# Optimization experiments

Hardware: AMD Instinct MI355X
Metric: run time of the kernel (lower is better)

The kernel has to match this reference:

```python
import jax, jax.numpy as jnp
import numpy as np

N = 2048          # num_nodes
A = 100           # anchor count (hard-coded in _select_anchor_points)


def setup_inputs() -> dict:
    key = jax.random.key(0)
    k1, k2, k3 = jax.random.split(key, 3)
    motifGraph = jax.random.uniform(k1, (N, N), dtype=jnp.float32)
    node_weights = jax.random.uniform(k2, (N,), dtype=jnp.float32)
    weight_matrix = jax.random.uniform(k3, (N, A), dtype=jnp.float32)
    sigma = jnp.array(1.0, dtype=jnp.float32)
    return {"motifGraph": motifGraph, "node_weights": node_weights,
            "weight_matrix": weight_matrix, "sigma": sigma}


def _floyd_warshall(w):
    # w: [n,n] edge-weight matrix (inf = no edge, 0 on diagonal)
    n = w.shape[0]
    def step(d, k):
        # d_ij = min(d_ij, d_ik + d_kj)
        d = jnp.minimum(d, d[:, k][:, None] + d[k, :][None, :])
        return d, None
    d, _ = jax.lax.scan(step, w, jnp.arange(n))
    return d


def reference(motifGraph, node_weights, weight_matrix, sigma):
    n = motifGraph.shape[0]
    # _adjust_motif_graph: row-scale by node weights. The original detaches
    # before the scipy floyd_warshall call, so no grad flows through it.
    adj = jax.lax.stop_gradient(motifGraph * node_weights[:n, None])
    # csr_matrix semantics: zero entries are "no edge"; directed=False takes
    # the min of w_ij and w_ji; diagonal distance is 0.
    w = jnp.where(adj > 0, adj, jnp.inf)
    w = jnp.minimum(w, w.T)
    idx = jnp.arange(n)
    w = w.at[idx, idx].set(0.0)
    dist = _floyd_warshall(w)
    dist = jnp.where(jnp.isinf(dist), 100.0, dist)
    # _select_anchor_points: top-100 node weights (all indices < n here)
    anchors = jnp.argsort(-jax.lax.stop_gradient(node_weights))[:A]
    consensus_vectors = dist[:, anchors]                      # [n, A]
    distance_sums = (consensus_vectors.sum(axis=1) - 100.0).sum() / (n * A)
    weighted = weight_matrix[:n, :] * consensus_vectors       # [n, A]
    # build_consensus_graph: cdist(...)**4 == (squared euclidean dist)**2
    xx = jnp.sum(weighted * weighted, axis=1)                 # [n]
    sq = jnp.maximum(xx[:, None] + xx[None, :] - 2.0 * weighted @ weighted.T, 0.0)
    consensus_graph = jnp.exp(-(sq * sq) / (2.0 * sigma ** 2))
    return consensus_vectors, distance_sums, consensus_graph
```

## Files before the change

### kernel.cpp

```cpp
#include <hip/hip_runtime.h>
#include <stdint.h>

#define NN 2048
#define AA 100
#define NT 32

#define F_DIAG 256
#define F_ROW  512
#define F_COL  1536

typedef float floatx4 __attribute__((ext_vector_type(4)));

template<bool AL> __device__ __forceinline__ float4 ld4(const float* __restrict__ p) {
  if (AL) return *(const float4*)p;
  return make_float4(p[0], p[1], p[2], p[3]);
}
template<bool AL> __device__ __forceinline__ void st4(float* __restrict__ p, float4 v) {
  if (AL) { *(float4*)p = v; }
  else { p[0] = v.x; p[1] = v.y; p[2] = v.z; p[3] = v.w; }
}

__device__ __forceinline__ void minplus16(const float (*A)[68], const float (*B)[68],
                                          float c[4][4], int i0, int j0) {
#pragma unroll 4
  for (int k4 = 0; k4 < 16; ++k4) {
    const int k = k4 * 4;
    float4 a0 = *(const float4*)&A[i0 + 0][k];
    float4 a1 = *(const float4*)&A[i0 + 1][k];
    float4 a2 = *(const float4*)&A[i0 + 2][k];
    float4 a3 = *(const float4*)&A[i0 + 3][k];
    float4 b0 = *(const float4*)&B[k + 0][j0];
    float4 b1 = *(const float4*)&B[k + 1][j0];
    float4 b2 = *(const float4*)&B[k + 2][j0];
    float4 b3 = *(const float4*)&B[k + 3][j0];
#define MP1(ii, jj, f)                                                           \
    c[ii][jj] = fminf(fminf(fminf(fminf(c[ii][jj], a##ii.x + b0.f),              \
                                  a##ii.y + b1.f),                               \
                            a##ii.z + b2.f),                                     \
                      a##ii.w + b3.f)
#define MP_ROW(ii) MP1(ii, 0, x); MP1(ii, 1, y); MP1(ii, 2, z); MP1(ii, 3, w)
    MP_ROW(0); MP_ROW(1); MP_ROW(2); MP_ROW(3);
#undef MP_ROW
#undef MP1
  }
}

__device__ __forceinline__ void close_seq(float (*S)[68], float c[4][4],
                                          int i0, int j0, int ty, int tx) {
  for (int kb = 0; kb < 16; ++kb) {
#pragma unroll
    for (int h = 0; h < 2; ++h) {
      const int k = kb * 4 + h * 2;
      float4 br  = *(const float4*)&S[k][j0];
      float4 br2 = *(const float4*)&S[k + 1][j0];
      float dkk1 = S[k][k + 1];
      float dk1k = S[k + 1][k];
      float a0 = S[i0 + 0][k],     a1 = S[i0 + 1][k],
            a2 = S[i0 + 2][k],     a3 = S[i0 + 3][k];
      float e0 = S[i0 + 0][k + 1], e1 = S[i0 + 1][k + 1],
            e2 = S[i0 + 2][k + 1], e3 = S[i0 + 3][k + 1];
      float4 brp;
      brp.x = fminf(br2.x, dk1k + br.x);
      brp.y = fminf(br2.y, dk1k + br.y);
      brp.z = fminf(br2.z, dk1k + br.z);
      brp.w = fminf(br2.w, dk1k + br.w);
      e0 = fminf(e0, a0 + dkk1);
      e1 = fminf(e1, a1 + dkk1);
      e2 = fminf(e2, a2 + dkk1);
      e3 = fminf(e3, a3 + dkk1);
#define CS2(ii, aa, ee)                                                     \
      c[ii][0] = fminf(fminf(c[ii][0], aa + br.x), ee + brp.x);             \
      c[ii][1] = fminf(fminf(c[ii][1], aa + br.y), ee + brp.y);             \
      c[ii][2] = fminf(fminf(c[ii][2], aa + br.z), ee + brp.z);             \
      c[ii][3] = fminf(fminf(c[ii][3], aa + br.w), ee + brp.w)
      CS2(0, a0, e0); CS2(1, a1, e1); CS2(2, a2, e2); CS2(3, a3, e3);
#undef CS2
      const int kn = k + 2;
      if (kn < 64) {
        const int ow = kn >> 2;
        const int ri = (h == 0) ? 2 : 0;
        if (ow == ty) {
          *(float4*)&S[kn][j0] =
              make_float4(c[ri][0], c[ri][1], c[ri][2], c[ri][3]);
          *(float4*)&S[kn + 1][j0] =
              make_float4(c[ri + 1][0], c[ri + 1][1], c[ri + 1][2], c[ri + 1][3]);
        }
        if (ow == tx) {
          S[i0 + 0][kn] = c[0][ri]; S[i0 + 0][kn + 1] = c[0][ri + 1];
          S[i0 + 1][kn] = c[1][ri]; S[i0 + 1][kn + 1] = c[1][ri + 1];
          S[i0 + 2][kn] = c[2][ri]; S[i0 + 2][kn + 1] = c[2][ri + 1];
          S[i0 + 3][kn] = c[3][ri]; S[i0 + 3][kn + 1] = c[3][ri + 1];
        }
      }
      __syncthreads();
    }
  }
}

template<int LAZY>
__device__ __forceinline__ void waitflag(int* f) {
  int it = 0;
  while (__hip_atomic_load(f, __ATOMIC_RELAXED, __HIP_MEMORY_SCOPE_AGENT) == 0) {
    if (++it > 24) __builtin_amdgcn_s_sleep(LAZY);
  }
}
__device__ __forceinline__ void setflag(int* f) {
  __hip_atomic_store(f, 1, __ATOMIC_RELAXED, __HIP_MEMORY_SCOPE_AGENT);
}

__device__ __forceinline__ void stage64(const float* __restrict__ g,
                                        float (*S)[68], int t) {
#pragma unroll
  for (int l = 0; l < 4; ++l) {
    int idx = l * 256 + t;
    int row = idx >> 4, c4 = (idx & 15) * 4;
    *(float4*)&S[row][c4] = *(const float4*)&g[row * 64 + c4];
  }
}
__device__ __forceinline__ void pub64_wt(float* __restrict__ g,
                                         const float c[4][4], int i0, int j0) {
#pragma unroll
  for (int ii = 0; ii < 4; ++ii) {
    floatx4 v = {c[ii][0], c[ii][1], c[ii][2], c[ii][3]};
    float* p = &g[(i0 + ii) * 64 + j0];
    asm volatile("global_store_dwordx4 %0, %1, off sc0 sc1"
                 :: "v"(p), "v"(v) : "memory");
  }
  asm volatile("s_waitcnt vmcnt(0)" ::: "memory");
}

__global__ __launch_bounds__(256, 4) void fw_persist(
    const float* __restrict__ mg, const float* __restrict__ nw,
    float* __restrict__ dist, int* __restrict__ Wi,
    float* __restrict__ diagb, float* __restrict__ rowb,
    float* __restrict__ colb) {
  __shared__ __align__(16) float As[64][68];
  __shared__ __align__(16) float Bs[64][68];
  const int bx = blockIdx.x, by = blockIdx.y;
  const int t = threadIdx.x;
  const int tx = t & 15, ty = t >> 4;
  const int i0 = ty * 4, j0 = tx * 4;
  int* DIAGF = Wi + F_DIAG;
  int* ROWF  = Wi + F_ROW;
  int* COLF  = Wi + F_COL;

#pragma unroll
  for (int l = 0; l < 4; ++l) {
    int idx = l * 256 + t;
    int r = idx >> 4, c4 = (idx & 15) * 4;
    float4 g = *(const float4*)&mg[(bx * 64 + r) * NN + by * 64 + c4];
    Bs[c4 + 0][r] = g.x; Bs[c4 + 1][r] = g.y;
    Bs[c4 + 2][r] = g.z; Bs[c4 + 3][r] = g.w;
  }
  __syncthreads();
  float c[4][4];
  {
    float4 nwj = *(const float4*)&nw[bx * 64 + j0];
#pragma unroll
    for (int ii = 0; ii < 4; ++ii) {
      int rl = i0 + ii;
      int i = by * 64 + rl;
      float nwi = nw[i];
      float4 m = *(const float4*)&mg[i * NN + bx * 64 + j0];
      float4 bt = *(const float4*)&Bs[rl][j0];
      float av[4] = {m.x * nwi, m.y * nwi, m.z * nwi, m.w * nwi};
      float bv[4] = {bt.x * nwj.x, bt.y * nwj.y, bt.z * nwj.z, bt.w * nwj.w};
#pragma unroll
      for (int q = 0; q < 4; ++q) {
        float wa = av[q] > 0.0f ? av[q] : __builtin_huge_valf();
        float wb = bv[q] > 0.0f ? bv[q] : __builtin_huge_valf();
        float v = fminf(wa, wb);
        if (i == bx * 64 + j0 + q) v = 0.0f;
        c[ii][q] = v;
      }
    }
  }
  if (bx == 0 && by == 0) {
    __syncthreads();
#pragma unroll
    for (int ii = 0; ii < 4; ++ii)
      *(float4*)&As[i0 + ii][j0] = make_float4(c[ii][0], c[ii][1], c[ii][2], c[ii][3]);
    __syncthreads();
    close_seq(As, c, i0, j0, ty, tx);
    pub64_wt(diagb, c, i0, j0);
    __syncthreads();
    if (t == 0) setflag(DIAGF + 0);
  }

  for (int r = 0; r < NT; ++r) {
    const bool crit = (by == r) || (bx == r) || (by == r + 1) || (bx == r + 1);
    if (crit) __builtin_amdgcn_s_setprio(1);
    else      __builtin_amdgcn_s_setprio(0);
    if (by == r && bx == r) continue;
    if (by == r || bx == r) {
      const bool isRow = (by == r);
      __syncthreads();
      float (*Ow)[68] = isRow ? Bs : As;
#pragma unroll
      for (int ii = 0; ii < 4; ++ii)
        *(float4*)&Ow[i0 + ii][j0] =
            make_float4(c[ii][0], c[ii][1], c[ii][2], c[ii][3]);
      if (t == 0) waitflag<1>(DIAGF + r);
      __syncthreads();
      stage64(diagb + r * 4096, isRow ? As : Bs, t);
      __syncthreads();
      minplus16(As, Bs, c, i0, j0);
      float* ob = isRow ? rowb + (r * NT + bx) * 4096
                        : colb + (by * NT + r) * 4096;
      pub64_wt(ob, c, i0, j0);
      __syncthreads();
      if (t == 0) setflag(isRow ? ROWF + r * NT + bx : COLF + by * NT + r);
    } else {
      const bool closer = (bx == r + 1) && (by == r + 1) && (r + 1 < NT);
      if (t == 0) {
        if (crit) {
          waitflag<1>(ROWF + r * NT + bx);
          waitflag<1>(COLF + by * NT + r);
        } else {
          waitflag<8>(ROWF + r * NT + bx);
          waitflag<8>(COLF + by * NT + r);
        }
      }
      __syncthreads();
      stage64(colb + (by * NT + r) * 4096, As, t);
      stage64(rowb + (r * NT + bx) * 4096, Bs, t);
      __syncthreads();
      minplus16(As, Bs, c, i0, j0);
      if (closer) {
        __syncthreads();
#pragma unroll
        for (int ii = 0; ii < 4; ++ii)
          *(float4*)&As[i0 + ii][j0] =
              make_float4(c[ii][0], c[ii][1], c[ii][2], c[ii][3]);
        __syncthreads();
        close_seq(As, c, i0, j0, ty, tx);
        pub64_wt(diagb + (r + 1) * 4096, c, i0, j0);
        __syncthreads();
        if (t == 0) setflag(DIAGF + r + 1);
      }
    }
  }
  __builtin_amdgcn_s_setprio(0);

  float* ob = &dist[(by * 64) * NN + bx * 64];
#pragma unroll
  for (int ii = 0; ii < 4; ++ii)
    *(float4*)&ob[(i0 + ii) * NN + j0] =
        make_float4(c[ii][0], c[ii][1], c[ii][2], c[ii][3]);
}

template<bool AL>
__global__ __launch_bounds__(256) void build_w_kernel(
    const float* __restrict__ mg, const float* __restrict__ nw,
    float* __restrict__ w) {
  __shared__ float Tt[64][65];
  __shared__ __align__(16) float As[64][68];
  int bi = blockIdx.y, bj = blockIdx.x;
  int t = threadIdx.x;
  const bool diag0 = (bi == 0) && (bj == 0);
#pragma unroll
  for (int l = 0; l < 4; ++l) {
    int idx = l * 256 + t;
    int r = idx >> 4, c4 = (idx & 15) * 4;
    float4 g = *(const float4*)&mg[(bj * 64 + r) * NN + bi * 64 + c4];
    Tt[c4 + 0][r] = g.x; Tt[c4 + 1][r] = g.y;
    Tt[c4 + 2][r] = g.z; Tt[c4 + 3][r] = g.w;
  }
  __syncthreads();
#pragma unroll
  for (int l = 0; l < 4; ++l) {
    int idx = l * 256 + t;
    int r = idx >> 4, c4 = (idx & 15) * 4;
    int i = bi * 64 + r, j = bj * 64 + c4;
    float4 m = *(const float4*)&mg[i * NN + j];
    float4 nwj = *(const float4*)&nw[j];
    float nwi = nw[i];
    float av[4] = {m.x * nwi, m.y * nwi, m.z * nwi, m.w * nwi};
    float bv[4] = {Tt[r][c4 + 0] * nwj.x, Tt[r][c4 + 1] * nwj.y,
                   Tt[r][c4 + 2] * nwj.z, Tt[r][c4 + 3] * nwj.w};
    float vv[4];
#pragma unroll
    for (int q = 0; q < 4; ++q) {
      float wa = av[q] > 0.0f ? av[q] : __builtin_huge_valf();
      float wb = bv[q] > 0.0f ? bv[q] : __builtin_huge_valf();
      float v = fminf(wa, wb);
      if (i == j + q) v = 0.0f;
      vv[q] = v;
    }
    float4 v4 = make_float4(vv[0], vv[1], vv[2], vv[3]);
    if (diag0) {
      *(float4*)&As[r][c4] = v4;
    } else {
      st4<AL>(&w[i * NN + j], v4);
    }
  }
  if (diag0) {
    __syncthreads();
    int tx = t & 15, ty = t >> 4;
    int i0 = ty * 4, j0 = tx * 4;
    float c[4][4];
#pragma unroll
    for (int ii = 0; ii < 4; ++ii) {
      float4 q = *(const float4*)&As[i0 + ii][j0];
      c[ii][0] = q.x; c[ii][1] = q.y; c[ii][2] = q.z; c[ii][3] = q.w;
    }
    close_seq(As, c, i0, j0, ty, tx);
#pragma unroll
    for (int ii = 0; ii < 4; ++ii)
      st4<AL>(&w[(i0 + ii) * NN + j0],
              make_float4(c[ii][0], c[ii][1], c[ii][2], c[ii][3]));
  }
}

template<bool AL>
__global__ __launch_bounds__(256) void fw_p2(float* __restrict__ d, int r) {
  __shared__ __align__(16) float As[64][68];
  __shared__ __align__(16) float Bs[64][68];
  int tile = blockIdx.x, side = blockIdx.y;
  if (tile == r) return;
  int t = threadIdx.x;
  int dbase = (r * 64) * NN + r * 64;
  int obase = (side == 0) ? (r * 64) * NN + tile * 64
                          : (tile * 64) * NN + r * 64;
  float (*Da)[68] = (side == 0) ? As : Bs;
  float (*Ow)[68] = (side == 0) ? Bs : As;
#pragma unroll
  for (int l = 0; l < 4; ++l) {
    int idx = l * 256 + t;
    int row = idx >> 4, c4 = (idx & 15) * 4;
    *(float4*)&Da[row][c4] = ld4<AL>(&d[dbase + row * NN + c4]);
    *(float4*)&Ow[row][c4] = ld4<AL>(&d[obase + row * NN + c4]);
  }
  int tx = t & 15, ty = t >> 4;
  int i0 = ty * 4, j0 = tx * 4;
  __syncthreads();
  float c[4][4];
#pragma unroll
  for (int ii = 0; ii < 4; ++ii) {
    float4 q = *(const float4*)&Ow[i0 + ii][j0];
    c[ii][0] = q.x; c[ii][1] = q.y; c[ii][2] = q.z; c[ii][3] = q.w;
  }
  minplus16(As, Bs, c, i0, j0);
#pragma unroll
  for (int ii = 0; ii < 4; ++ii)
    st4<AL>(&d[obase + (i0 + ii) * NN + j0],
            make_float4(c[ii][0], c[ii][1], c[ii][2], c[ii][3]));
}

template<bool AL>
__global__ __launch_bounds__(256) void fw_p3(float* __restrict__ d, int r) {
  __shared__ __align__(16) float As[64][68];
  __shared__ __align__(16) float Bs[64][68];
  int bx = blockIdx.x, by = blockIdx.y;
  if (bx == r || by == r) return;
  int t = threadIdx.x;
#pragma unroll
  for (int l = 0; l < 4; ++l) {
    int idx = l * 256 + t;
    int row = idx >> 4, c4 = (idx & 15) * 4;
    *(float4*)&As[row][c4] = ld4<AL>(&d[(by * 64 + row) * NN + r * 64 + c4]);
    *(float4*)&Bs[row][c4] = ld4<AL>(&d[(r * 64 + row) * NN + bx * 64 + c4]);
  }
  int tx = t & 15, ty = t >> 4;
  int i0 = ty * 4, j0 = tx * 4;
  int obase = (by * 64) * NN + bx * 64;
  float c[4][4];
#pragma unroll
  for (int ii = 0; ii < 4; ++ii) {
    float4 q = ld4<AL>(&d[obase + (i0 + ii) * NN + j0]);
    c[ii][0] = q.x; c[ii][1] = q.y; c[ii][2] = q.z; c[ii][3] = q.w;
  }
  __syncthreads();
  minplus16(As, Bs, c, i0, j0);

  bool closer = (bx == r + 1) && (by == r + 1) && (r + 1 < NT);
  if (closer) {
    __syncthreads();
#pragma unroll
    for (int ii = 0; ii < 4; ++ii)
      *(float4*)&As[i0 + ii][j0] = make_float4(c[ii][0], c[ii][1], c[ii][2], c[ii][3]);
    __syncthreads();
    close_seq(As, c, i0, j0, ty, tx);
  }
#pragma unroll
  for (int ii = 0; ii < 4; ++ii)
    st4<AL>(&d[obase + (i0 + ii) * NN + j0],
            make_float4(c[ii][0], c[ii][1], c[ii][2], c[ii][3]));
}

__global__ __launch_bounds__(256) void anchors_kernel(
    const float* __restrict__ nw, int* __restrict__ anchors) {
  __shared__ __align__(16) float s[NN];
  int t = threadIdx.x;
#pragma unroll
  for (int l = 0; l < NN / 256; ++l) s[l * 256 + t] = nw[l * 256 + t];
  __syncthreads();
  int i = blockIdx.x * 64 + (t >> 2);
  int q = t & 3;
  float wi = s[i];
  int rank = 0;
  int jb = q * (NN / 4);
  for (int j = jb; j < jb + NN / 4; j += 4) {
    float4 v = *(const float4*)&s[j];
    rank += (int)(v.x > wi) + ((int)(v.x == wi) & (int)(j + 0 < i));
    rank += (int)(v.y > wi) + ((int)(v.y == wi) & (int)(j + 1 < i));
    rank += (int)(v.z > wi) + ((int)(v.z == wi) & (int)(j + 2 < i));
    rank += (int)(v.w > wi) + ((int)(v.w == wi) & (int)(j + 3 < i));
  }
  rank += __shfl_xor(rank, 1);
  rank += __shfl_xor(rank, 2);
  if (q == 0 && rank < AA) anchors[rank] = i;
}

__global__ __launch_bounds__(256) void cv_kernel(
    const float* __restrict__ dist, const int* __restrict__ anchors,
    float* __restrict__ cv_out, float* __restrict__ sum_acc) {
  int idx = blockIdx.x * 256 + threadIdx.x;
  int i = idx / 100, a = idx - i * 100;
  float dv = dist[i * NN + anchors[a]];
  if (isinf(dv)) dv = 100.0f;
  cv_out[idx] = dv;
  float v = dv;
#pragma unroll
  for (int off = 32; off > 0; off >>= 1) v += __shfl_down(v, off);
  __shared__ float sv[4];
  int lane = threadIdx.x & 63, w = threadIdx.x >> 6;
  if (lane == 0) sv[w] = v;
  __syncthreads();
  if (threadIdx.x == 0) atomicAdd(sum_acc, sv[0] + sv[1] + sv[2] + sv[3]);
}

__global__ __launch_bounds__(256) void graph_kernel(
    const float* __restrict__ wm, const float* __restrict__ cv,
    const float* __restrict__ sigma, float* __restrict__ graph) {
  __shared__ __align__(16) float As[64][108];
  __shared__ __align__(16) float Bs[64][108];
  __shared__ float xs[64], ys[64];
  int bx = blockIdx.x, by = blockIdx.y;
  int t = threadIdx.x;
#pragma unroll
  for (int l = 0; l < 7; ++l) {
    int idx = l * 256 + t;
    if (idx < 1600) {
      int row = idx / 25, c4 = (idx - row * 25) * 4;
      float4 wa = *(const float4*)&wm[(by * 64 + row) * AA + c4];
      float4 ca = *(const float4*)&cv[(by * 64 + row) * AA + c4];
      *(float4*)&As[row][c4] =
          make_float4(wa.x * ca.x, wa.y * ca.y, wa.z * ca.z, wa.w * ca.w);
      float4 wb = *(const float4*)&wm[(bx * 64 + row) * AA + c4];
      float4 cb = *(const float4*)&cv[(bx * 64 + row) * AA + c4];
      *(float4*)&Bs[row][c4] =
          make_float4(wb.x * cb.x, wb.y * cb.y, wb.z * cb.z, wb.w * cb.w);
    }
  }
  __syncthreads();
  if (t < 64) {
    float s = 0.0f;
    for (int k4 = 0; k4 < 25; ++k4) {
      float4 q = *(const float4*)&As[t][k4 * 4];
      s += q.x * q.x + q.y * q.y + q.z * q.z + q.w * q.w;
    }
    xs[t] = s;
  } else if (t < 128) {
    int r = t - 64;
    float s = 0.0f;
    for (int k4 = 0; k4 < 25; ++k4) {
      float4 q = *(const float4*)&Bs[r][k4 * 4];
      s += q.x * q.x + q.y * q.y + q.z * q.z + q.w * q.w;
    }
    ys[r] = s;
  }
  __syncthreads();
  int tx = t & 15, ty = t >> 4;
  float acc[4][4] = {{0.0f}};
#pragma unroll 5
  for (int k4 = 0; k4 < 25; ++k4) {
    int k = k4 * 4;
    float4 a_[4], b_[4];
#pragma unroll
    for (int ii = 0; ii < 4; ++ii) a_[ii] = *(const float4*)&As[ty + 16 * ii][k];
#pragma unroll
    for (int jj = 0; jj < 4; ++jj) b_[jj] = *(const float4*)&Bs[tx + 16 * jj][k];
#pragma unroll
    for (int ii = 0; ii < 4; ++ii)
#pragma unroll
      for (int jj = 0; jj < 4; ++jj)
        acc[ii][jj] += a_[ii].x * b_[jj].x + a_[ii].y * b_[jj].y +
                       a_[ii].z * b_[jj].z + a_[ii].w * b_[jj].w;
  }
  float s = *sigma;
  float inv2s2 = 0.5f / (s * s);
#pragma unroll
  for (int ii = 0; ii < 4; ++ii) {
    int gi = by * 64 + ty + 16 * ii;
    float xi = xs[ty + 16 * ii];
#pragma unroll
    for (int jj = 0; jj < 4; ++jj) {
      int gj = bx * 64 + tx + 16 * jj;
      float sq = fmaxf(xi + ys[tx + 16 * jj] - 2.0f * acc[ii][jj], 0.0f);
      graph[gi * NN + gj] = __expf(-(sq * sq) * inv2s2);
    }
  }
}

__global__ void finalize_kernel(const float* __restrict__ sum_acc,
                                float* __restrict__ out) {
  if (threadIdx.x == 0)
    *out = (*sum_acc - 204800.0f) / 204800.0f;
}

template<bool AL>
static void run_fw_fallback(const float* mg, const float* nw, float* dist,
                            hipStream_t stream) {
  build_w_kernel<AL><<<dim3(NT, NT), 256, 0, stream>>>(mg, nw, dist);
  for (int r = 0; r < NT; ++r) {
    fw_p2<AL><<<dim3(NT, 2), 256, 0, stream>>>(dist, r);
    fw_p3<AL><<<dim3(NT, NT), 256, 0, stream>>>(dist, r);
  }
}

static bool coop_ok() {
  static int ok = -1;
  if (ok < 0) {
    int dev = 0;
    (void)hipGetDevice(&dev);
    int coopAttr = 0;
    (void)hipDeviceGetAttribute(&coopAttr, hipDeviceAttributeCooperativeLaunch, dev);
    int cus = 0;
    (void)hipDeviceGetAttribute(&cus, hipDeviceAttributeMultiprocessorCount, dev);
    int nb = 0;
    hipError_t e = hipOccupancyMaxActiveBlocksPerMultiprocessor(&nb, fw_persist, 256, 0);
    ok = (e == hipSuccess && coopAttr && nb > 0 && (long)nb * cus >= NT * NT) ? 1 : 0;
  }
  return ok == 1;
}

extern "C" void kernel_launch(void* const* d_in, const int* in_sizes, int n_in,
                              void* d_out, int out_size, void* d_ws, size_t ws_size,
                              hipStream_t stream) {
  (void)in_sizes; (void)n_in; (void)out_size;
  const float* mg    = (const float*)d_in[0];
  const float* nw    = (const float*)d_in[1];
  const float* wm    = (const float*)d_in[2];
  const float* sigma = (const float*)d_in[3];
  float* out        = (float*)d_out;
  float* cv_out     = out;
  float* scalar_out = out + 204800;
  float* graph_out  = out + 204801;

  float* W = (float*)d_ws;
  float* sum_acc = W;
  int* anchors   = (int*)(W + 4);
  const size_t needP = (size_t)(16384 + (size_t)NN * NN + NT * 4096 +
                                2 * (size_t)NT * NT * 4096) * sizeof(float);
  const bool bigP  = ws_size >= needP;
  const bool bigF  = ws_size >= (size_t)(2048 + (size_t)NN * NN) * sizeof(float);
  float* dist = bigP ? (W + 16384) : (bigF ? (W + 2048) : graph_out);
  const bool al = ((((uintptr_t)dist) & 15) == 0);

  (void)hipMemsetAsync(W, 0, 16384, stream);

  bool launched = false;
  if (bigP && al && coop_ok()) {
    int* Wi = (int*)W;
    float* diagb = dist + (size_t)NN * NN;
    float* rowb  = diagb + NT * 4096;
    float* colb  = rowb + (size_t)NT * NT * 4096;
    void* args[] = {(void*)&mg, (void*)&nw, (void*)&dist, (void*)&Wi,
                    (void*)&diagb, (void*)&rowb, (void*)&colb};
    hipError_t ce = hipLaunchCooperativeKernel(fw_persist, dim3(NT, NT),
                                               dim3(256, 1, 1), args, 0, stream);
    launched = (ce == hipSuccess);
  }
  if (!launched) {
    if (al) run_fw_fallback<true>(mg, nw, dist, stream);
    else    run_fw_fallback<false>(mg, nw, dist, stream);
  }

  anchors_kernel<<<NN / 64, 256, 0, stream>>>(nw, anchors);
  cv_kernel<<<800, 256, 0, stream>>>(dist, anchors, cv_out, sum_acc);
  graph_kernel<<<dim3(NT, NT), 256, 0, stream>>>(wm, cv_out, sigma, graph_out);
  finalize_kernel<<<1, 64, 0, stream>>>(sum_acc, scalar_out);
}
```

Before: 921.7 us.

## Compute next diagonal tile's row/col dependencies locally to shorten critical path

New measurement: 951.1 us. 1.03x slower.

```diff
diff --git a/kernel.cpp b/kernel.cpp
--- a/kernel.cpp
+++ b/kernel.cpp
@@ -5,9 +5,11 @@
 #define AA 100
 #define NT 32
 
-#define F_DIAG 256
-#define F_ROW  512
-#define F_COL  1536
+#define F_DIAG   256
+#define F_ROW    512
+#define F_COL    1536
+#define F_PREROW 2560
+#define F_PRECOL 2624
 
 typedef float floatx4 __attribute__((ext_vector_type(4)));
 
@@ -133,16 +135,19 @@
     const float* __restrict__ mg, const float* __restrict__ nw,
     float* __restrict__ dist, int* __restrict__ Wi,
     float* __restrict__ diagb, float* __restrict__ rowb,
-    float* __restrict__ colb) {
+    float* __restrict__ colb, float* __restrict__ prerow,
+    float* __restrict__ precol) {
   __shared__ __align__(16) float As[64][68];
   __shared__ __align__(16) float Bs[64][68];
   const int bx = blockIdx.x, by = blockIdx.y;
   const int t = threadIdx.x;
   const int tx = t & 15, ty = t >> 4;
   const int i0 = ty * 4, j0 = tx * 4;
-  int* DIAGF = Wi + F_DIAG;
-  int* ROWF  = Wi + F_ROW;
-  int* COLF  = Wi + F_COL;
+  int* DIAGF   = Wi + F_DIAG;
+  int* ROWF    = Wi + F_ROW;
+  int* COLF    = Wi + F_COL;
+  int* PREROWF = Wi + F_PREROW;
+  int* PRECOLF = Wi + F_PRECOL;
 
 #pragma unroll
   for (int l = 0; l < 4; ++l) {
@@ -175,6 +180,11 @@
       }
     }
   }
+  if ((by == 0 && bx == 1) || (by == 1 && bx == 0)) {
+    pub64_wt((by == 0) ? prerow : precol, c, i0, j0);
+    __syncthreads();
+    if (t == 0) setflag((by == 0) ? PREROWF + 0 : PRECOLF + 0);
+  }
   if (bx == 0 && by == 0) {
     __syncthreads();
 #pragma unroll
@@ -192,7 +202,51 @@
     if (crit) __builtin_amdgcn_s_setprio(1);
     else      __builtin_amdgcn_s_setprio(0);
     if (by == r && bx == r) continue;
-    if (by == r || bx == r) {
+    const bool closer = (bx == r + 1) && (by == r + 1) && (r + 1 < NT);
+    if (closer) {
+      if (t == 0) {
+        waitflag<1>(DIAGF + r);
+        waitflag<1>(PREROWF + r);
+        waitflag<1>(PRECOLF + r);
+      }
+      __syncthreads();
+      stage64(precol + r * 4096, As, t);
+      stage64(diagb + r * 4096, Bs, t);
+      __syncthreads();
+      float cp[4][4], rp[4][4];
+#pragma unroll
+      for (int ii = 0; ii < 4; ++ii) {
+        float4 q = *(const float4*)&As[i0 + ii][j0];
+        cp[ii][0] = q.x; cp[ii][1] = q.y; cp[ii][2] = q.z; cp[ii][3] = q.w;
+      }
+      minplus16(As, Bs, cp, i0, j0);
+      __syncthreads();
+      stage64(prerow + r * 4096, As, t);
+      __syncthreads();
+#pragma unroll
+      for (int ii = 0; ii < 4; ++ii) {
+        float4 q = *(const float4*)&As[i0 + ii][j0];
+        rp[ii][0] = q.x; rp[ii][1] = q.y; rp[ii][2] = q.z; rp[ii][3] = q.w;
+      }
+      minplus16(Bs, As, rp, i0, j0);
+      __syncthreads();
+#pragma unroll
+      for (int ii = 0; ii < 4; ++ii) {
+        *(float4*)&As[i0 + ii][j0] = make_float4(cp[ii][0], cp[ii][1], cp[ii][2], cp[ii][3]);
+        *(float4*)&Bs[i0 + ii][j0] = make_float4(rp[ii][0], rp[ii][1], rp[ii][2], rp[ii][3]);
+      }
+      __syncthreads();
+      minplus16(As, Bs, c, i0, j0);
+      __syncthreads();
+#pragma unroll
+      for (int ii = 0; ii < 4; ++ii)
+        *(float4*)&As[i0 + ii][j0] = make_float4(c[ii][0], c[ii][1], c[ii][2], c[ii][3]);
+      __syncthreads();
+      close_seq(As, c, i0, j0, ty, tx);
+      pub64_wt(diagb + (r + 1) * 4096, c, i0, j0);
+      __syncthreads();
+      if (t == 0) setflag(DIAGF + r + 1);
+    } else if (by == r || bx == r) {
       const bool isRow = (by == r);
       __syncthreads();
       float (*Ow)[68] = isRow ? Bs : As;
@@ -211,7 +265,6 @@
       __syncthreads();
       if (t == 0) setflag(isRow ? ROWF + r * NT + bx : COLF + by * NT + r);
     } else {
-      const bool closer = (bx == r + 1) && (by == r + 1) && (r + 1 < NT);
       if (t == 0) {
         if (crit) {
           waitflag<1>(ROWF + r * NT + bx);
@@ -226,17 +279,16 @@
       stage64(rowb + (r * NT + bx) * 4096, Bs, t);
       __syncthreads();
       minplus16(As, Bs, c, i0, j0);
-      if (closer) {
-        __syncthreads();
-#pragma unroll
-        for (int ii = 0; ii < 4; ++ii)
-          *(float4*)&As[i0 + ii][j0] =
-              make_float4(c[ii][0], c[ii][1], c[ii][2], c[ii][3]);
-        __syncthreads();
-        close_seq(As, c, i0, j0, ty, tx);
-        pub64_wt(diagb + (r + 1) * 4096, c, i0, j0);
-        __syncthreads();
-        if (t == 0) setflag(DIAGF + r + 1);
+      if (r + 2 < NT) {
+        if (by == r + 1 && bx == r + 2) {
+          pub64_wt(prerow + (r + 1) * 4096, c, i0, j0);
+          __syncthreads();
+          if (t == 0) setflag(PREROWF + r + 1);
+        } else if (by == r + 2 && bx == r + 1) {
+          pub64_wt(precol + (r + 1) * 4096, c, i0, j0);
+          __syncthreads();
+          if (t == 0) setflag(PRECOLF + r + 1);
+        }
       }
     }
   }
@@ -551,7 +603,7 @@
   float* W = (float*)d_ws;
   float* sum_acc = W;
   int* anchors   = (int*)(W + 4);
-  const size_t needP = (size_t)(16384 + (size_t)NN * NN + NT * 4096 +
+  const size_t needP = (size_t)(16384 + (size_t)NN * NN + 3 * NT * 4096 +
                                 2 * (size_t)NT * NT * 4096) * sizeof(float);
   const bool bigP  = ws_size >= needP;
   const bool bigF  = ws_size >= (size_t)(2048 + (size_t)NN * NN) * sizeof(float);
@@ -563,11 +615,14 @@
   bool launched = false;
   if (bigP && al && coop_ok()) {
     int* Wi = (int*)W;
-    float* diagb = dist + (size_t)NN * NN;
-    float* rowb  = diagb + NT * 4096;
-    float* colb  = rowb + (size_t)NT * NT * 4096;
+    float* diagb  = dist + (size_t)NN * NN;
+    float* rowb   = diagb + NT * 4096;
+    float* colb   = rowb + (size_t)NT * NT * 4096;
+    float* prerow = colb + (size_t)NT * NT * 4096;
+    float* precol = prerow + NT * 4096;
     void* args[] = {(void*)&mg, (void*)&nw, (void*)&dist, (void*)&Wi,
-                    (void*)&diagb, (void*)&rowb, (void*)&colb};
+                    (void*)&diagb, (void*)&rowb, (void*)&colb,
+                    (void*)&prerow, (void*)&precol};
     hipError_t ce = hipLaunchCooperativeKernel(fw_persist, dim3(NT, NT),
                                                dim3(256, 1, 1), args, 0, stream);
     launched = (ce == hipSuccess);
```
